# Kernel tuning notes

Hardware: AMD Instinct MI355X
Metric: run time of the kernel (lower is better)

Reference implementation:

```python
import jax, jax.numpy as jnp
import numpy as np

N, E, G = 50000, 640000, 256
NODE_IN, EDGE_IN, H, L, T = 64, 16, 128, 4, 5
BN_EPS = 1e-5

def setup_inputs() -> dict:
    key = jax.random.key(0)
    ks = jax.random.split(key, 24)
    s = lambda k, shape, fan: jax.random.normal(k, shape, jnp.float32) * (1.0 / np.sqrt(fan))
    return {
        "x": jax.random.normal(ks[0], (N, NODE_IN), jnp.float32),
        "edge_attr": jax.random.normal(ks[1], (E, EDGE_IN), jnp.float32),
        "node_w": s(ks[2], (NODE_IN, H), NODE_IN), "node_b": jnp.zeros((H,), jnp.float32),
        "edge_w1": s(ks[3], (EDGE_IN, H), EDGE_IN), "edge_b1": jnp.zeros((H,), jnp.float32),
        "edge_w2": s(ks[4], (H, H), H), "edge_b2": jnp.zeros((H,), jnp.float32),
        "conv_w1": s(ks[5], (L, H, H), H), "conv_b1": jnp.zeros((L, H), jnp.float32),
        "conv_w2": s(ks[6], (L, H, H), H), "conv_b2": jnp.zeros((L, H), jnp.float32),
        "bn_gamma": jnp.ones((L, H), jnp.float32), "bn_beta": jnp.zeros((L, H), jnp.float32),
        "gate_w1": s(ks[7], (H, H // 2), H), "gate_b1": jnp.zeros((H // 2,), jnp.float32),
        "gate_w2": s(ks[8], (H // 2, 1), H // 2), "gate_b2": jnp.zeros((1,), jnp.float32),
        "head_w1": s(ks[9], (H, H), H), "head_b1": jnp.zeros((H,), jnp.float32),
        "head_w2": s(ks[10], (H, T), H), "head_b2": jnp.zeros((T,), jnp.float32),
        "edge_index": jax.random.randint(ks[11], (2, E), 0, N, jnp.int32),
        "batch": jnp.sort(jax.random.randint(ks[12], (N,), 0, G, jnp.int32)),
    }

def reference(x, edge_attr, node_w, node_b, edge_w1, edge_b1, edge_w2, edge_b2,
              conv_w1, conv_b1, conv_w2, conv_b2, bn_gamma, bn_beta,
              gate_w1, gate_b1, gate_w2, gate_b2, head_w1, head_b1, head_w2, head_b2,
              edge_index, batch):
    relu = jax.nn.relu
    h = x @ node_w + node_b                                   # [N,H]
    e = relu(edge_attr @ edge_w1 + edge_b1) @ edge_w2 + edge_b2  # [E,H]
    src, dst = edge_index[0], edge_index[1]
    bn_scale = 1.0 / jnp.sqrt(jnp.float32(1.0) + BN_EPS)      # eval BN: mean=0, var=1
    for l in range(L):
        m = relu(h[src] + e)                                  # GINEConv message [E,H]
        aggr = jax.ops.segment_sum(m, dst, num_segments=N)    # scatter-add
        z = h + aggr                                          # eps=0: (1+eps)*x + aggr
        z = relu(z @ conv_w1[l] + conv_b1[l]) @ conv_w2[l] + conv_b2[l]
        z = z * bn_scale * bn_gamma[l] + bn_beta[l]
        h = relu(z)                                           # dropout off (eval)
    gate = relu(h @ gate_w1 + gate_b1) @ gate_w2 + gate_b2    # [N,1]
    gmax = jax.ops.segment_max(gate, batch, num_segments=G)   # segment softmax
    wexp = jnp.exp(gate - gmax[batch])
    denom = jax.ops.segment_sum(wexp, batch, num_segments=G)
    alpha = wexp / denom[batch]
    g = jax.ops.segment_sum(alpha * h, batch, num_segments=G) # [G,H]
    return relu(g @ head_w1 + head_b1) @ head_w2 + head_b2    # [G,T]
```

## Files before the change

### kernel.cpp

```cpp
#include <hip/hip_runtime.h>

typedef unsigned short u16;
typedef __bf16 bf16x8 __attribute__((ext_vector_type(8)));
typedef __bf16 bf16x2 __attribute__((ext_vector_type(2)));
typedef float f32x4 __attribute__((ext_vector_type(4)));
typedef unsigned short u16x8 __attribute__((ext_vector_type(8)));

#define NNODES 50000
#define NEDGES 640000
#define NGRAPH 256
#define HCHUNK 4096
#define HSPLIT 64
#define NCHUNK 13

__device__ __forceinline__ float bf2f(u16 u) {
  unsigned int v = ((unsigned int)u) << 16; float f; __builtin_memcpy(&f, &v, 4); return f;
}
__device__ __forceinline__ u16 f2bf(float f) {
  unsigned int x; __builtin_memcpy(&x, &f, 4);
  unsigned int lsb = (x >> 16) & 1u;
  x += 0x7fffu + lsb;
  return (u16)(x >> 16);
}
__device__ __forceinline__ unsigned int pkbf(float a, float b) {
  bf16x2 p; p[0] = (__bf16)a; p[1] = (__bf16)b;
  unsigned int r; __builtin_memcpy(&r, &p, 4); return r;
}

__global__ void write_zero_f32(float* __restrict__ out, int n) {
  int i = blockIdx.x * 256 + threadIdx.x;
  if (i < n) out[i] = 0.f;
}

__global__ void prep_weights(const float* __restrict__ node_w, const float* __restrict__ edge_w1,
                             const float* __restrict__ edge_w2, const float* __restrict__ conv_w1,
                             const float* __restrict__ conv_w2, const float* __restrict__ gate_w1,
                             u16* __restrict__ node_wt, u16* __restrict__ edge_w1t,
                             u16* __restrict__ edge_w2t, u16* __restrict__ conv_w1t,
                             u16* __restrict__ conv_w2t, u16* __restrict__ gate_w1t) {
  int o = blockIdx.x * 256 + threadIdx.x;
  if (o < 8192) { int n = o >> 6, k = o & 63; node_wt[o] = f2bf(node_w[k * 128 + n]); return; }
  o -= 8192;
  if (o < 4096) { int n = o >> 5, k = o & 31;
                  edge_w1t[o] = (k < 16) ? f2bf(edge_w1[k * 128 + n]) : (u16)0; return; }
  o -= 4096;
  if (o < 16384) { int n = o >> 7, k = o & 127; edge_w2t[o] = f2bf(edge_w2[k * 128 + n]); return; }
  o -= 16384;
  if (o < 65536) { int l = o >> 14, r = o & 16383, n = r >> 7, k = r & 127;
                   conv_w1t[o] = f2bf(conv_w1[l * 16384 + k * 128 + n]); return; }
  o -= 65536;
  if (o < 65536) { int l = o >> 14, r = o & 16383, n = r >> 7, k = r & 127;
                   conv_w2t[o] = f2bf(conv_w2[l * 16384 + k * 128 + n]); return; }
  o -= 65536;
  if (o < 8192) { int n = o >> 7, k = o & 127; gate_w1t[o] = f2bf(gate_w1[k * 64 + n]); }
}

__global__ __launch_bounds__(256) void hist_k(const int* __restrict__ dst,
                                              int* __restrict__ partial) {
  __shared__ int hloc[HCHUNK];
  int b = blockIdx.x, t = threadIdx.x;
  int c = b >> 6, sp = b & 63;
  for (int j = t; j < HCHUNK; j += 256) hloc[j] = 0;
  __syncthreads();
  int base = c * HCHUNK;
  int e0 = sp * (NEDGES / HSPLIT), e1 = e0 + NEDGES / HSPLIT;
  for (int i = e0 + t; i < e1; i += 256) {
    int d = dst[i] - base;
    if ((unsigned)d < HCHUNK) atomicAdd(&hloc[d], 1);
  }
  __syncthreads();
  for (int j = t; j < HCHUNK; j += 256) {
    int g = base + j;
    if (g < NNODES) partial[(size_t)sp * NNODES + g] = hloc[j];
  }
}
__global__ __launch_bounds__(256) void scan_a(int* __restrict__ partial,
                                              int* __restrict__ counts,
                                              int* __restrict__ bsums,
                                              const int* __restrict__ batch,
                                              int* __restrict__ goffs, int n) {
  __shared__ int sh4[4];
  int b = blockIdx.x, t = threadIdx.x;
  int lane = t & 63, w = t >> 6;
  if (b == 49) {
    int lo = 0, hi = n;
    while (lo < hi) { int mid = (lo + hi) >> 1; if (batch[mid] < t) lo = mid + 1; else hi = mid; }
    goffs[t] = lo;
    if (t == 0) goffs[256] = n;
    return;
  }
  int i0 = b * 1024 + t * 4;
  int s = 0;
#pragma unroll
  for (int j = 0; j < 4; j++) {
    int g = i0 + j;
    if (g < n) {
      int run = 0;
      for (int sp = 0; sp < HSPLIT; sp++) {
        int v = partial[(size_t)sp * NNODES + g];
        partial[(size_t)sp * NNODES + g] = run;
        run += v;
      }
      counts[g] = run;
      s += run;
    }
  }
  for (int m = 32; m; m >>= 1) s += __shfl_xor(s, m, 64);
  if (lane == 0) sh4[w] = s;
  __syncthreads();
  if (t == 0) bsums[b] = sh4[0] + sh4[1] + sh4[2] + sh4[3];
}
__global__ __launch_bounds__(256) void scan_c(const int* __restrict__ counts,
                                              const int* __restrict__ bsums,
                                              int* __restrict__ offs, int n) {
  int b = blockIdx.x, t = threadIdx.x;
  int i0 = b * 1024 + t * 4;
  int v[4]; int s = 0;
#pragma unroll
  for (int j = 0; j < 4; j++) { v[j] = (i0 + j < n) ? counts[i0 + j] : 0; s += v[j]; }
  int lane = t & 63, w = t >> 6;
  int x = s;
  for (int d = 1; d < 64; d <<= 1) { int y = __shfl_up(x, (unsigned)d, 64); if (lane >= d) x += y; }
  __shared__ int wt_[4];
  if (lane == 63) wt_[w] = x;
  __syncthreads();
  int add = 0;
  for (int i = 0; i < b; i++) add += bsums[i];
  for (int i = 0; i < w; i++) add += wt_[i];
  int excl = add + x - s;
#pragma unroll
  for (int j = 0; j < 4; j++) {
    int i = i0 + j;
    if (i < n) offs[i] = excl;
    excl += v[j];
  }
  if (b == 0 && t == 0) offs[n] = NEDGES;
}
__global__ __launch_bounds__(256) void scatter_k(const int* __restrict__ src,
                                                 const int* __restrict__ dst,
                                                 const int* __restrict__ offs,
                                                 const int* __restrict__ partial,
                                                 int* __restrict__ csr_src,
                                                 int* __restrict__ csr_eid) {
  __shared__ int hloc[HCHUNK];
  int b = blockIdx.x, t = threadIdx.x;
  int c = b >> 6, sp = b & 63;
  for (int j = t; j < HCHUNK; j += 256) hloc[j] = 0;
  __syncthreads();
  int base = c * HCHUNK;
  int e0 = sp * (NEDGES / HSPLIT), e1 = e0 + NEDGES / HSPLIT;
  for (int i = e0 + t; i < e1; i += 256) {
    int d = dst[i];
    int dl = d - base;
    if ((unsigned)dl < HCHUNK) {
      int r = atomicAdd(&hloc[dl], 1);
      int p = offs[d] + partial[(size_t)sp * NNODES + d] + r;
      csr_src[p] = src[i];
      csr_eid[p] = i;
    }
  }
}

template <int KB, int SA, int SB>
__device__ __forceinline__ void mfma_block(const u16* aL, const u16* bL, int m, int quad,
                                           int rbase, f32x4* acc) {
#pragma unroll
  for (int kb = 0; kb < KB; ++kb) {
    bf16x8 a = *(const bf16x8*)(aL + (rbase + m) * SA + kb * 32 + quad * 8);
#pragma unroll
    for (int nt = 0; nt < 8; ++nt) {
      bf16x8 b = *(const bf16x8*)(bL + (nt * 16 + m) * SB + kb * 32 + quad * 8);
      acc[nt] = __builtin_amdgcn_mfma_f32_16x16x32_bf16(a, b, acc[nt], 0, 0, 0);
    }
  }
}

__global__ __launch_bounds__(256) void node_encode(const float* __restrict__ x,
                                                   const u16* __restrict__ wt,
                                                   const float* __restrict__ nb,
                                                   u16* __restrict__ hb, int n) {
  __shared__ alignas(16) u16 sA[64 * 72];
  __shared__ alignas(16) u16 sW[128 * 72];
  int t = threadIdx.x;
  int row0 = blockIdx.x * 64;
#pragma unroll
  for (int i = 0; i < 4; i++) {
    int idx = t + 256 * i; int r = idx >> 4, c = idx & 15;
    int grow = row0 + r; if (grow > n - 1) grow = n - 1;
    float4 v = *(const float4*)(x + (size_t)grow * 64 + c * 4);
    ushort4 o; o.x = f2bf(v.x); o.y = f2bf(v.y); o.z = f2bf(v.z); o.w = f2bf(v.w);
    *(ushort4*)&sA[r * 72 + c * 4] = o;
  }
#pragma unroll
  for (int i = 0; i < 4; i++) {
    int idx = t + 256 * i; int nr = idx >> 3, c = idx & 7;
    *(uint4*)&sW[nr * 72 + c * 8] = *(const uint4*)(wt + nr * 64 + c * 8);
  }
  __syncthreads();
  int lane = t & 63, w = t >> 6, m = lane & 15, quad = lane >> 4, rbase = w * 16;
  f32x4 acc[8];
  f32x4 z4 = {0.f, 0.f, 0.f, 0.f};
#pragma unroll
  for (int i = 0; i < 8; i++) acc[i] = z4;
  mfma_block<2, 72, 72>(sA, sW, m, quad, rbase, acc);
#pragma unroll
  for (int nt = 0; nt < 8; nt++) {
    int col = nt * 16 + m;
    float bb = nb[col];
    f32x4 a4 = acc[nt];
#pragma unroll
    for (int r = 0; r < 4; r++) {
      int grow = row0 + rbase + quad * 4 + r;
      if (grow < n) hb[(size_t)grow * 128 + col] = f2bf(a4[r] + bb);
    }
  }
}

__global__ __launch_bounds__(256) void edge_encode(const float* __restrict__ ea,
                                                   const u16* __restrict__ w1t,
                                                   const u16* __restrict__ w2t,
                                                   const float* __restrict__ b1,
                                                   const float* __restrict__ b2,
                                                   const int* __restrict__ csr_eid,
                                                   u16* __restrict__ e_perm) {
  __shared__ alignas(16) u16 sMid[128 * 132];
  int t = threadIdx.x;
  int lane = t & 63, w = t >> 6, m = lane & 15, quad = lane >> 4;
  int s0 = blockIdx.x * 128;
  int ebase = w * 32;

  int eidv = 0;
  if (lane < 32) eidv = csr_eid[s0 + ebase + lane];
  bf16x8 af[2];
#pragma unroll
  for (int rt2 = 0; rt2 < 2; rt2++) {
    int eid = __shfl(eidv, rt2 * 16 + m, 64);
    bf16x8 a = {};
    if (quad < 2) {
      float4 v0 = *(const float4*)(ea + (size_t)eid * 16 + quad * 8);
      float4 v1 = *(const float4*)(ea + (size_t)eid * 16 + quad * 8 + 4);
      a[0] = (__bf16)v0.x; a[1] = (__bf16)v0.y; a[2] = (__bf16)v0.z; a[3] = (__bf16)v0.w;
      a[4] = (__bf16)v1.x; a[5] = (__bf16)v1.y; a[6] = (__bf16)v1.z; a[7] = (__bf16)v1.w;
    }
    af[rt2] = a;
  }
  bf16x8 w1f[8];
#pragma unroll
  for (int nt = 0; nt < 8; nt++)
    w1f[nt] = *(const bf16x8*)(w1t + (nt * 16 + m) * 32 + quad * 8);

  f32x4 z4 = {0.f, 0.f, 0.f, 0.f};
  f32x4 acc1[16];
#pragma unroll
  for (int i = 0; i < 16; i++) acc1[i] = z4;
#pragma unroll
  for (int rt2 = 0; rt2 < 2; rt2++) {
#pragma unroll
    for (int nt = 0; nt < 8; nt++)
      acc1[rt2 * 8 + nt] = __builtin_amdgcn_mfma_f32_16x16x32_bf16(w1f[nt], af[rt2], acc1[rt2 * 8 + nt], 0, 0, 0);
  }
#pragma unroll
  for (int rt2 = 0; rt2 < 2; rt2++) {
#pragma unroll
    for (int nt = 0; nt < 8; nt++) {
      float4 bb = *(const float4*)&b1[nt * 16 + quad * 4];
      f32x4 a4 = acc1[rt2 * 8 + nt];
      uint2 pk;
      pk.x = pkbf(fmaxf(a4[0] + bb.x, 0.f), fmaxf(a4[1] + bb.y, 0.f));
      pk.y = pkbf(fmaxf(a4[2] + bb.z, 0.f), fmaxf(a4[3] + bb.w, 0.f));
      *(uint2*)&sMid[(ebase + rt2 * 16 + m) * 132 + nt * 16 + quad * 4] = pk;
    }
  }
  bf16x8 w2f[8];
  float4 b2v[2];
#pragma unroll
  for (int ct = 0; ct < 2; ct++) {
    b2v[ct] = *(const float4*)&b2[w * 32 + ct * 16 + quad * 4];
#pragma unroll
    for (int kb = 0; kb < 4; kb++)
      w2f[ct * 4 + kb] = *(const bf16x8*)(w2t + (size_t)(w * 32 + ct * 16 + m) * 128 + kb * 32 + quad * 8);
  }
  __syncthreads();

  f32x4 acc2[16];
#pragma unroll
  for (int i = 0; i < 16; i++) acc2[i] = z4;
#pragma unroll
  for (int rt = 0; rt < 8; rt++) {
#pragma unroll
    for (int kb = 0; kb < 4; kb++) {
      bf16x8 a = *(const bf16x8*)(&sMid[(rt * 16 + m) * 132 + kb * 32 + quad * 8]);
      acc2[rt * 2 + 0] = __builtin_amdgcn_mfma_f32_16x16x32_bf16(w2f[kb], a, acc2[rt * 2 + 0], 0, 0, 0);
      acc2[rt * 2 + 1] = __builtin_amdgcn_mfma_f32_16x16x32_bf16(w2f[4 + kb], a, acc2[rt * 2 + 1], 0, 0, 0);
    }
  }
  __syncthreads();
#pragma unroll
  for (int rt = 0; rt < 8; rt++) {
#pragma unroll
    for (int ct = 0; ct < 2; ct++) {
      f32x4 a4 = acc2[rt * 2 + ct];
      uint2 pk;
      pk.x = pkbf(a4[0] + b2v[ct].x, a4[1] + b2v[ct].y);
      pk.y = pkbf(a4[2] + b2v[ct].z, a4[3] + b2v[ct].w);
      *(uint2*)&sMid[(rt * 16 + m) * 132 + w * 32 + ct * 16 + quad * 4] = pk;
    }
  }
  __syncthreads();
#pragma unroll
  for (int i = 0; i < 8; i++) {
    int idx = t + 256 * i; int r = idx >> 4, c = idx & 15;
    *(uint4*)(e_perm + (size_t)(s0 + r) * 128 + c * 8) = *(const uint4*)&sMid[r * 132 + c * 8];
  }
}

template <bool GATE>
__global__ __launch_bounds__(256) void layer_k(const u16* __restrict__ hin,
                                               u16* __restrict__ hout,
                                               const u16* __restrict__ e_perm,
                                               const int* __restrict__ offs,
                                               const int* __restrict__ csr_src,
                                               const u16* __restrict__ w1t, const u16* __restrict__ w2t,
                                               const float* __restrict__ b1, const float* __restrict__ b2,
                                               const float* __restrict__ gam, const float* __restrict__ bet,
                                               const u16* __restrict__ gw1t, const float* __restrict__ gb1,
                                               const float* __restrict__ gw2, const float* __restrict__ gb2,
                                               float* __restrict__ gate_out, int n) {
  __shared__ alignas(16) u16 sZ[64 * 132];
  __shared__ alignas(16) u16 sMid[64 * 132];
  int t = threadIdx.x;
  int lane = t & 63, w = t >> 6, m = lane & 15, quad = lane >> 4;
  int row0 = blockIdx.x * 64;
  int li = m, q = quad;

  int oidx = row0 + w * 16 + (lane < 16 ? lane : 16);
  if (oidx > n) oidx = n;
  int offv = offs[oidx];

  for (int k = 0; k < 16; k++) {
    int nd = row0 + w * 16 + k;
    int ndc = (nd > n - 1) ? (n - 1) : nd;
    int e0 = __shfl(offv, k, 64), e1 = __shfl(offv, k + 1, 64);
    u16x8 hv = {};
    if (q == 0) hv = *(const u16x8*)(hin + (size_t)ndc * 128 + li * 8);
    float a[8];
#pragma unroll
    for (int j = 0; j < 8; j++) a[j] = 0.f;
    int s = e0 + q;
    for (; s + 8 <= e1; s += 8) {
      int v0 = csr_src[s], v1 = csr_src[s + 4];
      u16x8 h0 = *(const u16x8*)(hin + (size_t)v0 * 128 + li * 8);
      u16x8 ee0 = *(const u16x8*)(e_perm + (size_t)s * 128 + li * 8);
      u16x8 h1 = *(const u16x8*)(hin + (size_t)v1 * 128 + li * 8);
      u16x8 ee1 = *(const u16x8*)(e_perm + (size_t)(s + 4) * 128 + li * 8);
#pragma unroll
      for (int j = 0; j < 8; j++) {
        a[j] += fmaxf(bf2f(h0[j]) + bf2f(ee0[j]), 0.f);
        a[j] += fmaxf(bf2f(h1[j]) + bf2f(ee1[j]), 0.f);
      }
    }
    for (; s < e1; s += 4) {
      int v = csr_src[s];
      u16x8 hgv = *(const u16x8*)(hin + (size_t)v * 128 + li * 8);
      u16x8 ev = *(const u16x8*)(e_perm + (size_t)s * 128 + li * 8);
#pragma unroll
      for (int j = 0; j < 8; j++) a[j] += fmaxf(bf2f(hgv[j]) + bf2f(ev[j]), 0.f);
    }
#pragma unroll
    for (int j = 0; j < 8; j++) {
      a[j] += __shfl_xor(a[j], 16, 64);
      a[j] += __shfl_xor(a[j], 32, 64);
    }
    if (q == 0) {
      bf16x8 o;
#pragma unroll
      for (int j = 0; j < 8; j++) o[j] = (__bf16)(bf2f(hv[j]) + a[j]);
      *(bf16x8*)&sZ[(w * 16 + k) * 132 + li * 8] = o;
    }
  }
  bf16x8 w1f[8];
  float4 b1v[2];
#pragma unroll
  for (int ct = 0; ct < 2; ct++) {
    b1v[ct] = *(const float4*)&b1[w * 32 + ct * 16 + quad * 4];
#pragma unroll
    for (int kb = 0; kb < 4; kb++)
      w1f[ct * 4 + kb] = *(const bf16x8*)(w1t + (size_t)(w * 32 + ct * 16 + m) * 128 + kb * 32 + quad * 8);
  }
  __syncthreads();

  f32x4 z4 = {0.f, 0.f, 0.f, 0.f};
  f32x4 acc[8];
#pragma unroll
  for (int i = 0; i < 8; i++) acc[i] = z4;
#pragma unroll
  for (int rt = 0; rt < 4; rt++) {
#pragma unroll
    for (int kb = 0; kb < 4; kb++) {
      bf16x8 a = *(const bf16x8*)(&sZ[(rt * 16 + m) * 132 + kb * 32 + quad * 8]);
      acc[rt * 2 + 0] = __builtin_amdgcn_mfma_f32_16x16x32_bf16(w1f[kb], a, acc[rt * 2 + 0], 0, 0, 0);
      acc[rt * 2 + 1] = __builtin_amdgcn_mfma_f32_16x16x32_bf16(w1f[4 + kb], a, acc[rt * 2 + 1], 0, 0, 0);
    }
  }
#pragma unroll
  for (int rt = 0; rt < 4; rt++) {
#pragma unroll
    for (int ct = 0; ct < 2; ct++) {
      f32x4 a4 = acc[rt * 2 + ct];
      uint2 pk;
      pk.x = pkbf(fmaxf(a4[0] + b1v[ct].x, 0.f), fmaxf(a4[1] + b1v[ct].y, 0.f));
      pk.y = pkbf(fmaxf(a4[2] + b1v[ct].z, 0.f), fmaxf(a4[3] + b1v[ct].w, 0.f));
      *(uint2*)&sMid[(rt * 16 + m) * 132 + w * 32 + ct * 16 + quad * 4] = pk;
    }
  }
  bf16x8 w2f[8];
  float4 b2v[2], gamv[2], betv[2];
#pragma unroll
  for (int ct = 0; ct < 2; ct++) {
    int c0 = w * 32 + ct * 16 + quad * 4;
    b2v[ct] = *(const float4*)&b2[c0];
    gamv[ct] = *(const float4*)&gam[c0];
    betv[ct] = *(const float4*)&bet[c0];
#pragma unroll
    for (int kb = 0; kb < 4; kb++)
      w2f[ct * 4 + kb] = *(const bf16x8*)(w2t + (size_t)(w * 32 + ct * 16 + m) * 128 + kb * 32 + quad * 8);
  }
  __syncthreads();

  f32x4 acc2[8];
#pragma unroll
  for (int i = 0; i < 8; i++) acc2[i] = z4;
#pragma unroll
  for (int rt = 0; rt < 4; rt++) {
#pragma unroll
    for (int kb = 0; kb < 4; kb++) {
      bf16x8 a = *(const bf16x8*)(&sMid[(rt * 16 + m) * 132 + kb * 32 + quad * 8]);
      acc2[rt * 2 + 0] = __builtin_amdgcn_mfma_f32_16x16x32_bf16(w2f[kb], a, acc2[rt * 2 + 0], 0, 0, 0);
      acc2[rt * 2 + 1] = __builtin_amdgcn_mfma_f32_16x16x32_bf16(w2f[4 + kb], a, acc2[rt * 2 + 1], 0, 0, 0);
    }
  }
  const float bns = 0.99999500003749983f;
#pragma unroll
  for (int rt = 0; rt < 4; rt++) {
#pragma unroll
    for (int ct = 0; ct < 2; ct++) {
      f32x4 a4 = acc2[rt * 2 + ct];
      uint2 pk;
      pk.x = pkbf(fmaxf((a4[0] + b2v[ct].x) * bns * gamv[ct].x + betv[ct].x, 0.f),
                  fmaxf((a4[1] + b2v[ct].y) * bns * gamv[ct].y + betv[ct].y, 0.f));
      pk.y = pkbf(fmaxf((a4[2] + b2v[ct].z) * bns * gamv[ct].z + betv[ct].z, 0.f),
                  fmaxf((a4[3] + b2v[ct].w) * bns * gamv[ct].w + betv[ct].w, 0.f));
      *(uint2*)&sZ[(rt * 16 + m) * 132 + w * 32 + ct * 16 + quad * 4] = pk;
    }
  }
  __syncthreads();
#pragma unroll
  for (int i = 0; i < 4; i++) {
    int idx = t + 256 * i; int r = idx >> 4, c = idx & 15;
    int grow = row0 + r;
    if (grow < n)
      *(uint4*)(hout + (size_t)grow * 128 + c * 8) = *(const uint4*)&sZ[r * 132 + c * 8];
  }

  if (GATE) {
    int rbase = w * 16;
    f32x4 gacc[4];
#pragma unroll
    for (int i = 0; i < 4; i++) gacc[i] = z4;
#pragma unroll
    for (int kb = 0; kb < 4; kb++) {
      bf16x8 a = *(const bf16x8*)(&sZ[(rbase + m) * 132 + kb * 32 + quad * 8]);
#pragma unroll
      for (int nt = 0; nt < 4; nt++) {
        bf16x8 b = *(const bf16x8*)(gw1t + (nt * 16 + m) * 128 + kb * 32 + quad * 8);
        gacc[nt] = __builtin_amdgcn_mfma_f32_16x16x32_bf16(a, b, gacc[nt], 0, 0, 0);
      }
    }
    float gb1v[4], gw2v[4];
#pragma unroll
    for (int nt = 0; nt < 4; nt++) { gb1v[nt] = gb1[nt * 16 + m]; gw2v[nt] = gw2[nt * 16 + m]; }
    float gb2v = gb2[0];
#pragma unroll
    for (int r = 0; r < 4; r++) {
      float p = 0.f;
#pragma unroll
      for (int nt = 0; nt < 4; nt++) p += fmaxf(gacc[nt][r] + gb1v[nt], 0.f) * gw2v[nt];
      p += __shfl_xor(p, 1, 64);
      p += __shfl_xor(p, 2, 64);
      p += __shfl_xor(p, 4, 64);
      p += __shfl_xor(p, 8, 64);
      if (m == 0) {
        int grow = row0 + rbase + quad * 4 + r;
        if (grow < n) gate_out[grow] = p + gb2v;
      }
    }
  }
}

__global__ __launch_bounds__(256) void pool_head_k(const float* __restrict__ gate,
                                                   const u16* __restrict__ hb,
                                                   const int* __restrict__ goffs,
                                                   const float* __restrict__ hw1,
                                                   const float* __restrict__ hb1,
                                                   const float* __restrict__ hw2,
                                                   const float* __restrict__ hb2,
                                                   float* __restrict__ out) {
  int g = blockIdx.x, t = threadIdx.x;
  int s0 = goffs[g], s1 = goffs[g + 1];
  int lane = t & 63, w = t >> 6;
  __shared__ float red[4];
  __shared__ float fin[2][128];
  __shared__ float shid[128];
  float mx = -3.4e38f;
  for (int i = s0 + t; i < s1; i += 256) mx = fmaxf(mx, gate[i]);
  for (int d = 32; d; d >>= 1) mx = fmaxf(mx, __shfl_xor(mx, d, 64));
  if (lane == 0) red[w] = mx;
  __syncthreads();
  mx = fmaxf(fmaxf(red[0], red[1]), fmaxf(red[2], red[3]));
  __syncthreads();
  float sm = 0.f;
  for (int i = s0 + t; i < s1; i += 256) sm += __expf(gate[i] - mx);
  for (int d = 32; d; d >>= 1) sm += __shfl_xor(sm, d, 64);
  if (lane == 0) red[w] = sm;
  __syncthreads();
  sm = red[0] + red[1] + red[2] + red[3];
  int g2 = t >> 7, tc = t & 127;
  float acc = 0.f;
  for (int i = s0 + g2; i < s1; i += 2)
    acc += __expf(gate[i] - mx) * bf2f(hb[(size_t)i * 128 + tc]);
  fin[g2][tc] = acc;
  __syncthreads();
  if (t < 128) fin[0][t] = (s1 > s0) ? (fin[0][t] + fin[1][t]) / sm : 0.f;
  __syncthreads();
  if (t < 128) {
    float s = 0.f;
    for (int k = 0; k < 128; k++) s += fin[0][k] * hw1[k * 128 + t];
    shid[t] = fmaxf(s + hb1[t], 0.f);
  }
  __syncthreads();
  if (t < 5) {
    float o = hb2[t];
    for (int k = 0; k < 128; k++) o += shid[k] * hw2[k * 5 + t];
    out[g * 5 + t] = o;
  }
}

extern "C" void kernel_launch(void* const* d_in, const int* in_sizes, int n_in,
                              void* d_out, int out_size, void* d_ws, size_t ws_size,
                              hipStream_t stream) {
  const int N = NNODES, E = NEDGES, G = NGRAPH;
  const float* x = (const float*)d_in[0];
  const float* edge_attr = (const float*)d_in[1];
  const float* node_w = (const float*)d_in[2];
  const float* node_b = (const float*)d_in[3];
  const float* edge_w1 = (const float*)d_in[4];
  const float* edge_b1 = (const float*)d_in[5];
  const float* edge_w2 = (const float*)d_in[6];
  const float* edge_b2 = (const float*)d_in[7];
  const float* conv_w1 = (const float*)d_in[8];
  const float* conv_b1 = (const float*)d_in[9];
  const float* conv_w2 = (const float*)d_in[10];
  const float* conv_b2 = (const float*)d_in[11];
  const float* bn_gamma = (const float*)d_in[12];
  const float* bn_beta = (const float*)d_in[13];
  const float* gate_w1 = (const float*)d_in[14];
  const float* gate_b1 = (const float*)d_in[15];
  const float* gate_w2 = (const float*)d_in[16];
  const float* gate_b2 = (const float*)d_in[17];
  const float* head_w1 = (const float*)d_in[18];
  const float* head_b1 = (const float*)d_in[19];
  const float* head_w2 = (const float*)d_in[20];
  const float* head_b2 = (const float*)d_in[21];
  const int* eidx = (const int*)d_in[22];
  const int* batch = (const int*)d_in[23];
  const int* esrc = eidx;
  const int* edst = eidx + E;

  char* wp = (char*)d_ws;
  auto alloc = [&](size_t bytes) { char* p = wp; wp += (bytes + 255) & ~(size_t)255; return p; };
  u16* e_perm = (u16*)alloc((size_t)E * 128 * 2);
  u16* hb = (u16*)alloc((size_t)(N + 16) * 128 * 2);
  u16* hb2 = (u16*)alloc((size_t)(N + 16) * 128 * 2);
  float* gate = (float*)alloc((size_t)N * 4);
  int* counts = (int*)alloc((size_t)N * 4);
  int* offs = (int*)alloc((size_t)(N + 1) * 4);
  int* partial = (int*)alloc((size_t)HSPLIT * N * 4);
  int* csr_src = (int*)alloc((size_t)E * 4);
  int* csr_eid = (int*)alloc((size_t)E * 4);
  int* bsums = (int*)alloc(64 * 4);
  int* goffs = (int*)alloc((G + 1) * 4);
  u16* node_wt = (u16*)alloc(8192 * 2);
  u16* edge_w1t = (u16*)alloc(4096 * 2);
  u16* edge_w2t = (u16*)alloc(16384 * 2);
  u16* conv_w1t = (u16*)alloc(65536 * 2);
  u16* conv_w2t = (u16*)alloc(65536 * 2);
  u16* gate_w1t = (u16*)alloc(8192 * 2);

  size_t need = (size_t)(wp - (char*)d_ws);
  if (need > ws_size) {
    write_zero_f32<<<(out_size + 255) / 256, 256, 0, stream>>>((float*)d_out, out_size);
    return;
  }

  prep_weights<<<656, 256, 0, stream>>>(node_w, edge_w1, edge_w2, conv_w1, conv_w2, gate_w1,
                                        node_wt, edge_w1t, edge_w2t, conv_w1t, conv_w2t, gate_w1t);
  hist_k<<<NCHUNK * HSPLIT, 256, 0, stream>>>(edst, partial);
  scan_a<<<50, 256, 0, stream>>>(partial, counts, bsums, batch, goffs, N);
  scan_c<<<49, 256, 0, stream>>>(counts, bsums, offs, N);
  scatter_k<<<NCHUNK * HSPLIT, 256, 0, stream>>>(esrc, edst, offs, partial, csr_src, csr_eid);
  node_encode<<<(N + 63) / 64, 256, 0, stream>>>(x, node_wt, node_b, hb, N);
  edge_encode<<<E / 128, 256, 0, stream>>>(edge_attr, edge_w1t, edge_w2t, edge_b1, edge_b2,
                                           csr_eid, e_perm);
  u16* hcur = hb;
  u16* hnext = hb2;
  for (int l = 0; l < 4; l++) {
    if (l < 3)
      layer_k<false><<<(N + 63) / 64, 256, 0, stream>>>(hcur, hnext, e_perm, offs, csr_src,
                                                        conv_w1t + l * 16384, conv_w2t + l * 16384,
                                                        conv_b1 + l * 128, conv_b2 + l * 128,
                                                        bn_gamma + l * 128, bn_beta + l * 128,
                                                        gate_w1t, gate_b1, gate_w2, gate_b2,
                                                        (float*)nullptr, N);
    else
      layer_k<true><<<(N + 63) / 64, 256, 0, stream>>>(hcur, hnext, e_perm, offs, csr_src,
                                                       conv_w1t + l * 16384, conv_w2t + l * 16384,
                                                       conv_b1 + l * 128, conv_b2 + l * 128,
                                                       bn_gamma + l * 128, bn_beta + l * 128,
                                                       gate_w1t, gate_b1, gate_w2, gate_b2,
                                                       gate, N);
    u16* tmp = hcur; hcur = hnext; hnext = tmp;
  }
  pool_head_k<<<G, 256, 0, stream>>>(gate, hcur, goffs, head_w1, head_b1, head_w2, head_b2,
                                     (float*)d_out);
}
```

Measured before the change: 597.2 us.

## Gather one node per lane group in layer_k and widen CSR scan grids

```diff
diff --git a/kernel.cpp b/kernel.cpp
--- a/kernel.cpp
+++ b/kernel.cpp
@@ -82,30 +82,25 @@
   __shared__ int sh4[4];
   int b = blockIdx.x, t = threadIdx.x;
   int lane = t & 63, w = t >> 6;
-  if (b == 49) {
+  if (b == 196) {
     int lo = 0, hi = n;
     while (lo < hi) { int mid = (lo + hi) >> 1; if (batch[mid] < t) lo = mid + 1; else hi = mid; }
     goffs[t] = lo;
     if (t == 0) goffs[256] = n;
     return;
   }
-  int i0 = b * 1024 + t * 4;
-  int s = 0;
-#pragma unroll
-  for (int j = 0; j < 4; j++) {
-    int g = i0 + j;
-    if (g < n) {
-      int run = 0;
-      for (int sp = 0; sp < HSPLIT; sp++) {
-        int v = partial[(size_t)sp * NNODES + g];
-        partial[(size_t)sp * NNODES + g] = run;
-        run += v;
-      }
-      counts[g] = run;
-      s += run;
-    }
-  }
-  for (int m = 32; m; m >>= 1) s += __shfl_xor(s, m, 64);
+  int g = b * 256 + t;
+  int run = 0;
+  if (g < n) {
+    for (int sp = 0; sp < HSPLIT; sp++) {
+      int v = partial[(size_t)sp * NNODES + g];
+      partial[(size_t)sp * NNODES + g] = run;
+      run += v;
+    }
+    counts[g] = run;
+  }
+  int s = run;
+  for (int mm = 32; mm; mm >>= 1) s += __shfl_xor(s, mm, 64);
   if (lane == 0) sh4[w] = s;
   __syncthreads();
   if (t == 0) bsums[b] = sh4[0] + sh4[1] + sh4[2] + sh4[3];
@@ -113,27 +108,27 @@
 __global__ __launch_bounds__(256) void scan_c(const int* __restrict__ counts,
                                               const int* __restrict__ bsums,
                                               int* __restrict__ offs, int n) {
+  __shared__ int sh4[4];
+  __shared__ int wt_[4];
+  __shared__ int base_sh;
   int b = blockIdx.x, t = threadIdx.x;
-  int i0 = b * 1024 + t * 4;
-  int v[4]; int s = 0;
-#pragma unroll
-  for (int j = 0; j < 4; j++) { v[j] = (i0 + j < n) ? counts[i0 + j] : 0; s += v[j]; }
   int lane = t & 63, w = t >> 6;
-  int x = s;
-  for (int d = 1; d < 64; d <<= 1) { int y = __shfl_up(x, (unsigned)d, 64); if (lane >= d) x += y; }
-  __shared__ int wt_[4];
-  if (lane == 63) wt_[w] = x;
-  __syncthreads();
-  int add = 0;
-  for (int i = 0; i < b; i++) add += bsums[i];
+  int v = (t < b) ? bsums[t] : 0;
+  int sv = v;
+  for (int mm = 32; mm; mm >>= 1) sv += __shfl_xor(sv, mm, 64);
+  if (lane == 0) sh4[w] = sv;
+  __syncthreads();
+  if (t == 0) base_sh = sh4[0] + sh4[1] + sh4[2] + sh4[3];
+  int g = b * 256 + t;
+  int x = (g < n) ? counts[g] : 0;
+  int inc = x;
+  for (int d = 1; d < 64; d <<= 1) { int y = __shfl_up(inc, (unsigned)d, 64); if (lane >= d) inc += y; }
+  if (lane == 63) wt_[w] = inc;
+  __syncthreads();
+  int add = base_sh;
   for (int i = 0; i < w; i++) add += wt_[i];
-  int excl = add + x - s;
-#pragma unroll
-  for (int j = 0; j < 4; j++) {
-    int i = i0 + j;
-    if (i < n) offs[i] = excl;
-    excl += v[j];
-  }
+  int excl = add + inc - x;
+  if (g < n) offs[g] = excl;
   if (b == 0 && t == 0) offs[n] = NEDGES;
 }
 __global__ __launch_bounds__(256) void scatter_k(const int* __restrict__ src,
@@ -331,52 +326,45 @@
   int t = threadIdx.x;
   int lane = t & 63, w = t >> 6, m = lane & 15, quad = lane >> 4;
   int row0 = blockIdx.x * 64;
-  int li = m, q = quad;
+  int li = m;
 
   int oidx = row0 + w * 16 + (lane < 16 ? lane : 16);
   if (oidx > n) oidx = n;
   int offv = offs[oidx];
 
-  for (int k = 0; k < 16; k++) {
-    int nd = row0 + w * 16 + k;
+  for (int k = 0; k < 4; k++) {
+    int lr = w * 16 + quad * 4 + k;
+    int nd = row0 + lr;
     int ndc = (nd > n - 1) ? (n - 1) : nd;
-    int e0 = __shfl(offv, k, 64), e1 = __shfl(offv, k + 1, 64);
-    u16x8 hv = {};
-    if (q == 0) hv = *(const u16x8*)(hin + (size_t)ndc * 128 + li * 8);
+    int e0 = __shfl(offv, quad * 4 + k, 64), e1 = __shfl(offv, quad * 4 + k + 1, 64);
+    u16x8 hv = *(const u16x8*)(hin + (size_t)ndc * 128 + li * 8);
     float a[8];
 #pragma unroll
     for (int j = 0; j < 8; j++) a[j] = 0.f;
-    int s = e0 + q;
-    for (; s + 8 <= e1; s += 8) {
-      int v0 = csr_src[s], v1 = csr_src[s + 4];
+    int s = e0;
+    for (; s + 2 <= e1; s += 2) {
+      int v0 = csr_src[s], v1 = csr_src[s + 1];
       u16x8 h0 = *(const u16x8*)(hin + (size_t)v0 * 128 + li * 8);
       u16x8 ee0 = *(const u16x8*)(e_perm + (size_t)s * 128 + li * 8);
       u16x8 h1 = *(const u16x8*)(hin + (size_t)v1 * 128 + li * 8);
-      u16x8 ee1 = *(const u16x8*)(e_perm + (size_t)(s + 4) * 128 + li * 8);
+      u16x8 ee1 = *(const u16x8*)(e_perm + (size_t)(s + 1) * 128 + li * 8);
 #pragma unroll
       for (int j = 0; j < 8; j++) {
         a[j] += fmaxf(bf2f(h0[j]) + bf2f(ee0[j]), 0.f);
         a[j] += fmaxf(bf2f(h1[j]) + bf2f(ee1[j]), 0.f);
       }
     }
-    for (; s < e1; s += 4) {
+    if (s < e1) {
       int v = csr_src[s];
       u16x8 hgv = *(const u16x8*)(hin + (size_t)v * 128 + li * 8);
       u16x8 ev = *(const u16x8*)(e_perm + (size_t)s * 128 + li * 8);
 #pragma unroll
       for (int j = 0; j < 8; j++) a[j] += fmaxf(bf2f(hgv[j]) + bf2f(ev[j]), 0.f);
     }
-#pragma unroll
-    for (int j = 0; j < 8; j++) {
-      a[j] += __shfl_xor(a[j], 16, 64);
-      a[j] += __shfl_xor(a[j], 32, 64);
-    }
-    if (q == 0) {
-      bf16x8 o;
-#pragma unroll
-      for (int j = 0; j < 8; j++) o[j] = (__bf16)(bf2f(hv[j]) + a[j]);
-      *(bf16x8*)&sZ[(w * 16 + k) * 132 + li * 8] = o;
-    }
+    bf16x8 o;
+#pragma unroll
+    for (int j = 0; j < 8; j++) o[j] = (__bf16)(bf2f(hv[j]) + a[j]);
+    *(bf16x8*)&sZ[lr * 132 + li * 8] = o;
   }
   bf16x8 w1f[8];
   float4 b1v[2];
@@ -587,7 +575,7 @@
   int* partial = (int*)alloc((size_t)HSPLIT * N * 4);
   int* csr_src = (int*)alloc((size_t)E * 4);
   int* csr_eid = (int*)alloc((size_t)E * 4);
-  int* bsums = (int*)alloc(64 * 4);
+  int* bsums = (int*)alloc(256 * 4);
   int* goffs = (int*)alloc((G + 1) * 4);
   u16* node_wt = (u16*)alloc(8192 * 2);
   u16* edge_w1t = (u16*)alloc(4096 * 2);
@@ -605,8 +593,8 @@
   prep_weights<<<656, 256, 0, stream>>>(node_w, edge_w1, edge_w2, conv_w1, conv_w2, gate_w1,
                                         node_wt, edge_w1t, edge_w2t, conv_w1t, conv_w2t, gate_w1t);
   hist_k<<<NCHUNK * HSPLIT, 256, 0, stream>>>(edst, partial);
-  scan_a<<<50, 256, 0, stream>>>(partial, counts, bsums, batch, goffs, N);
-  scan_c<<<49, 256, 0, stream>>>(counts, bsums, offs, N);
+  scan_a<<<197, 256, 0, stream>>>(partial, counts, bsums, batch, goffs, N);
+  scan_c<<<196, 256, 0, stream>>>(counts, bsums, offs, N);
   scatter_k<<<NCHUNK * HSPLIT, 256, 0, stream>>>(esrc, edst, offs, partial, csr_src, csr_eid);
   node_encode<<<(N + 63) / 64, 256, 0, stream>>>(x, node_wt, node_b, hb, N);
   edge_encode<<<E / 128, 256, 0, stream>>>(edge_attr, edge_w1t, edge_w2t, edge_b1, edge_b2,
```

After: 566.3 us. 1.05x faster.
